# Kernel optimization log

Hardware: AMD Instinct MI355X
Metric: run time of the kernel (lower is better)

Reference implementation:

```python
import jax, jax.numpy as jnp
import numpy as np

N_NODES = 50000
N_EDGES = 800000
IN_FEATS = 128
N_HEADS = 4
OUT_FEATS = 32
NEG_SLOPE = 0.01  # F.leaky_relu default


def setup_inputs() -> dict:
    key = jax.random.key(0)
    k1, k2, k3, k4, k5, k6 = jax.random.split(key, 6)
    feat = jax.random.normal(k1, (N_NODES, IN_FEATS), dtype=jnp.float32)
    src = jax.random.randint(k2, (N_EDGES,), 0, N_NODES, dtype=jnp.int64)
    dst = jax.random.randint(k3, (N_EDGES,), 0, N_NODES, dtype=jnp.int64)
    # xavier-ish scaled params
    W_fc = jax.random.normal(k4, (IN_FEATS, N_HEADS * OUT_FEATS), dtype=jnp.float32) * 0.1
    attn_l = jax.random.normal(k5, (N_HEADS, OUT_FEATS), dtype=jnp.float32) * 0.1
    attn_r = jax.random.normal(k6, (N_HEADS, OUT_FEATS), dtype=jnp.float32) * 0.1
    return {"feat": feat, "src": src, "dst": dst, "W_fc": W_fc,
            "attn_l": attn_l, "attn_r": attn_r}


def reference(feat, src, dst, W_fc, attn_l, attn_r):
    N = feat.shape[0]
    H, D = attn_l.shape
    # fc projection -> [N, H, D]
    h = (feat @ W_fc).reshape(N, H, D)
    # per-node attention logits [N, H]
    el = jnp.einsum('nhd,hd->nh', h, attn_l)
    er = jnp.einsum('nhd,hd->nh', h, attn_r)
    # edge scores: u_add_v then leaky_relu -> [E, H]
    e = jax.nn.leaky_relu(el[src] + er[dst], NEG_SLOPE)
    # faithful to torch.softmax(e, dim=1): softmax over the HEADS axis per edge
    a = jax.nn.softmax(e, axis=1)
    # weighted messages and sum-aggregation over destination nodes
    msg = h[src] * a[:, :, None]                     # [E, H, D]
    rst = jax.ops.segment_sum(msg, dst, num_segments=N)  # [N, H, D]
    # residual: res_fc is Identity since in_feats == H*D
    rst = rst + feat.reshape(N, H, D)
    return jax.nn.elu(rst)
```

## Files before the change

kernel.cpp:

```cpp
#include <hip/hip_runtime.h>

typedef float f32x4 __attribute__((ext_vector_type(4)));
typedef __bf16 bf16x8 __attribute__((ext_vector_type(8)));
typedef unsigned short u16x4 __attribute__((ext_vector_type(4)));
typedef unsigned short u16x8 __attribute__((ext_vector_type(8)));

#define BSH 4
#define BN 16
#define CAPFIX 512
#define PNB_MAX 3200
#define PCH 4096
#define FC_ROWS 64

__device__ inline unsigned short f2bf(float x) {
  unsigned int u = __builtin_bit_cast(unsigned int, x);
  unsigned int r = (u + 0x7FFFu + ((u >> 16) & 1u)) >> 16;
  return (unsigned short)r;
}
__device__ inline float bf2f(unsigned short h) {
  unsigned int u = ((unsigned int)h) << 16;
  return __builtin_bit_cast(float, u);
}

__global__ __launch_bounds__(256) void zero_kernel(int* __restrict__ p, int n) {
  int i = blockIdx.x * 256 + threadIdx.x;
  if (i < n) p[i] = 0;
}

__device__ void partition_body(char* smem, const int* __restrict__ src,
                               const int* __restrict__ dst,
                               int* __restrict__ bcursor, int* __restrict__ tmp,
                               int E, int nbuck, int blk) {
  int* cnt = (int*)smem;
  int* lcur = cnt + PNB_MAX;
  int t = threadIdx.x;
  int base = blk * PCH;
  for (int i = t; i < nbuck; i += 256) cnt[i] = 0;
  __syncthreads();
  int rec[16];
  int bb[16];
#pragma unroll
  for (int i = 0; i < 16; ++i) {
    int e = base + t + i * 256;
    bb[i] = -1;
    if (e < E) {
      int d = dst[e];
      int b = d >> BSH;
      bb[i] = b;
      rec[i] = (src[e] & 0xFFFF) | ((d & (BN - 1)) << 16);
      atomicAdd(&cnt[b], 1);
    }
  }
  __syncthreads();
  for (int i = t; i < nbuck; i += 256) {
    int c = cnt[i];
    lcur[i] = c ? atomicAdd(&bcursor[i], c) : 0;
  }
  __syncthreads();
#pragma unroll
  for (int i = 0; i < 16; ++i) {
    if (bb[i] >= 0) {
      int p = atomicAdd(&lcur[bb[i]], 1);
      if (p < CAPFIX) tmp[(size_t)bb[i] * CAPFIX + p] = rec[i];
    }
  }
}

__device__ void fc_body(char* smem, const float* __restrict__ feat,
                        const float* __restrict__ W,
                        const float* __restrict__ al, const float* __restrict__ ar,
                        unsigned short* __restrict__ hbf,
                        float* __restrict__ el, float* __restrict__ er,
                        int N, int blk) {
  unsigned short* Wbl = (unsigned short*)smem;
  unsigned short* Albs = (unsigned short*)(smem + 32768);
  int t = threadIdx.x;
  int row0 = blk * FC_ROWS;
#pragma unroll
  for (int i = 0; i < 8; ++i) {
    int ch = i * 256 + t;
    int col = ch & 127;
    int kg = ch >> 7;
    float v[8];
#pragma unroll
    for (int j = 0; j < 8; ++j) v[j] = W[(kg * 8 + j) * 128 + col];
    int scol = col ^ ((kg & 7) << 4);
    u16x8 pk = {f2bf(v[0]), f2bf(v[1]), f2bf(v[2]), f2bf(v[3]),
                f2bf(v[4]), f2bf(v[5]), f2bf(v[6]), f2bf(v[7])};
    *(u16x8*)&Wbl[(size_t)(kg * 128 + scol) * 8] = pk;
  }
#pragma unroll
  for (int i = 0; i < 4; ++i) {
    int ch = i * 256 + t;
    int row = ch >> 4;
    int kg = ch & 15;
    int grow = row0 + row;
    f32x4 x0 = {}, x1 = {};
    if (grow < N) {
      const f32x4* fp = (const f32x4*)(feat + (size_t)grow * 128 + kg * 8);
      x0 = fp[0];
      x1 = fp[1];
    }
    int sc = kg * 64 + (row ^ kg);
    u16x8 pk = {f2bf(x0[0]), f2bf(x0[1]), f2bf(x0[2]), f2bf(x0[3]),
                f2bf(x1[0]), f2bf(x1[1]), f2bf(x1[2]), f2bf(x1[3])};
    *(u16x8*)&Albs[sc * 8] = pk;
  }
  __syncthreads();
  int w = t >> 6;
  int l = t & 63;
  int lr = l & 15;
  int lhi = l >> 4;
  f32x4 acc[8] = {};
  bf16x8 afr[4];
#pragma unroll
  for (int ks = 0; ks < 4; ++ks) {
    int kg = ks * 4 + lhi;
    int row = w * 16 + lr;
    afr[ks] = *(const bf16x8*)&Albs[(kg * 64 + (row ^ kg)) * 8];
  }
#pragma unroll
  for (int nt = 0; nt < 8; ++nt) {
#pragma unroll
    for (int ks = 0; ks < 4; ++ks) {
      int kg = ks * 4 + lhi;
      int col = nt * 16 + lr;
      int scol = col ^ ((kg & 7) << 4);
      bf16x8 b = *(const bf16x8*)&Wbl[(size_t)(kg * 128 + scol) * 8];
      acc[nt] = __builtin_amdgcn_mfma_f32_16x16x32_bf16(afr[ks], b, acc[nt], 0, 0, 0);
    }
  }
#pragma unroll
  for (int nt = 0; nt < 8; ++nt) {
#pragma unroll
    for (int r = 0; r < 4; ++r) {
      int g = row0 + w * 16 + lhi * 4 + r;
      if (g < N) hbf[(size_t)g * 128 + nt * 16 + lr] = f2bf(acc[nt][r]);
    }
  }
  f32x4 pl[4] = {}, pr[4] = {};
#pragma unroll
  for (int nt = 0; nt < 8; ++nt) {
    int hd = nt >> 1;
    float wl = al[nt * 16 + lr];
    float wr = ar[nt * 16 + lr];
#pragma unroll
    for (int r = 0; r < 4; ++r) {
      pl[r][hd] += acc[nt][r] * wl;
      pr[r][hd] += acc[nt][r] * wr;
    }
  }
#pragma unroll
  for (int off = 1; off < 16; off <<= 1) {
#pragma unroll
    for (int r = 0; r < 4; ++r) {
#pragma unroll
      for (int c = 0; c < 4; ++c) {
        pl[r][c] += __shfl_xor(pl[r][c], off);
        pr[r][c] += __shfl_xor(pr[r][c], off);
      }
    }
  }
  if (lr == 0) {
#pragma unroll
    for (int r = 0; r < 4; ++r) {
      int g = row0 + w * 16 + lhi * 4 + r;
      if (g < N) *(f32x4*)(el + (size_t)g * 4) = pl[r];
    }
  } else if (lr == 1) {
#pragma unroll
    for (int r = 0; r < 4; ++r) {
      int g = row0 + w * 16 + lhi * 4 + r;
      if (g < N) *(f32x4*)(er + (size_t)g * 4) = pr[r];
    }
  }
}

__global__ __launch_bounds__(256) void fused_pfc(const int* __restrict__ src,
                                                 const int* __restrict__ dst,
                                                 int* __restrict__ bcursor,
                                                 int* __restrict__ tmp,
                                                 const float* __restrict__ feat,
                                                 const float* __restrict__ W,
                                                 const float* __restrict__ al,
                                                 const float* __restrict__ ar,
                                                 unsigned short* __restrict__ hbf,
                                                 float* __restrict__ el,
                                                 float* __restrict__ er,
                                                 int E, int N, int nbuck, int npart) {
  __shared__ alignas(16) char smem[49152];
  if ((int)blockIdx.x < npart)
    partition_body(smem, src, dst, bcursor, tmp, E, nbuck, blockIdx.x);
  else
    fc_body(smem, feat, W, al, ar, hbf, el, er, N, blockIdx.x - npart);
}

__global__ __launch_bounds__(256) void bucket_gather(const unsigned short* __restrict__ hbf,
                                                     const float* __restrict__ el,
                                                     const float* __restrict__ er,
                                                     const int* __restrict__ bcnt,
                                                     const int* __restrict__ tmp,
                                                     const float* __restrict__ feat,
                                                     float* __restrict__ out, int N) {
  __shared__ unsigned short as_s[CAPFIX];
  __shared__ unsigned short as_a[CAPFIX * 4];
  __shared__ f32x4 er_l[BN];
  __shared__ int cnt[BN], lb[BN], lc2[BN];
  int t = threadIdx.x;
  int bkt = blockIdx.x;
  int nstart = bkt << BSH;
  if (t < BN) {
    int nd = nstart + t;
    f32x4 e4 = {};
    if (nd < N) e4 = *(const f32x4*)(er + (size_t)nd * 4);
    er_l[t] = e4;
    cnt[t] = 0;
    lc2[t] = 0;
  }
  __syncthreads();
  int nrec = min(bcnt[bkt], CAPFIX);
  int myrec[2], mydlo[2];
#pragma unroll
  for (int i = 0; i < 2; ++i) {
    int idx = t + i * 256;
    mydlo[i] = -1;
    if (idx < nrec) {
      int r = tmp[(size_t)bkt * CAPFIX + idx];
      myrec[i] = r;
      int dlo = (r >> 16) & (BN - 1);
      mydlo[i] = dlo;
      atomicAdd(&cnt[dlo], 1);
    }
  }
  __syncthreads();
  if (t < BN) {
    int v = cnt[t];
    int s = v;
#pragma unroll
    for (int o = 1; o < BN; o <<= 1) {
      int x = __shfl_up(s, o, BN);
      if (t >= o) s += x;
    }
    lb[t] = s - v;
  }
  __syncthreads();
#pragma unroll
  for (int i = 0; i < 2; ++i) {
    if (mydlo[i] >= 0) {
      int r = myrec[i];
      int s = r & 0xFFFF;
      int dlo = mydlo[i];
      int p = lb[dlo] + atomicAdd(&lc2[dlo], 1);
      f32x4 l4 = *(const f32x4*)(el + (size_t)s * 4);
      f32x4 r4 = er_l[dlo];
      float e0 = l4[0] + r4[0];
      float e1 = l4[1] + r4[1];
      float e2 = l4[2] + r4[2];
      float e3 = l4[3] + r4[3];
      e0 = e0 > 0.f ? e0 : 0.01f * e0;
      e1 = e1 > 0.f ? e1 : 0.01f * e1;
      e2 = e2 > 0.f ? e2 : 0.01f * e2;
      e3 = e3 > 0.f ? e3 : 0.01f * e3;
      float m = fmaxf(fmaxf(e0, e1), fmaxf(e2, e3));
      float a0 = __expf(e0 - m);
      float a1 = __expf(e1 - m);
      float a2 = __expf(e2 - m);
      float a3 = __expf(e3 - m);
      float inv = 1.0f / (a0 + a1 + a2 + a3);
      u16x4 a = {f2bf(a0 * inv), f2bf(a1 * inv), f2bf(a2 * inv), f2bf(a3 * inv)};
      as_s[p] = (unsigned short)s;
      *(u16x4*)&as_a[p * 4] = a;
    }
  }
  __syncthreads();
  int gid = t >> 5, lane = t & 31, head = lane >> 3;
#pragma unroll
  for (int ni = 0; ni < 2; ++ni) {
    int g = gid * 2 + ni;
    int nd = nstart + g;
    f32x4 acc = {};
    int st = lb[g], en = st + cnt[g];
    int e = st;
    for (; e + 3 < en; e += 4) {
      int s0 = as_s[e + 0];
      int s1 = as_s[e + 1];
      int s2 = as_s[e + 2];
      int s3 = as_s[e + 3];
      float a0 = bf2f(as_a[(e + 0) * 4 + head]);
      float a1 = bf2f(as_a[(e + 1) * 4 + head]);
      float a2 = bf2f(as_a[(e + 2) * 4 + head]);
      float a3 = bf2f(as_a[(e + 3) * 4 + head]);
      u16x4 v0 = *(const u16x4*)&hbf[(size_t)s0 * 128 + lane * 4];
      u16x4 v1 = *(const u16x4*)&hbf[(size_t)s1 * 128 + lane * 4];
      u16x4 v2 = *(const u16x4*)&hbf[(size_t)s2 * 128 + lane * 4];
      u16x4 v3 = *(const u16x4*)&hbf[(size_t)s3 * 128 + lane * 4];
      f32x4 h0 = {bf2f(v0[0]), bf2f(v0[1]), bf2f(v0[2]), bf2f(v0[3])};
      f32x4 h1 = {bf2f(v1[0]), bf2f(v1[1]), bf2f(v1[2]), bf2f(v1[3])};
      f32x4 h2 = {bf2f(v2[0]), bf2f(v2[1]), bf2f(v2[2]), bf2f(v2[3])};
      f32x4 h3 = {bf2f(v3[0]), bf2f(v3[1]), bf2f(v3[2]), bf2f(v3[3])};
      acc += h0 * a0;
      acc += h1 * a1;
      acc += h2 * a2;
      acc += h3 * a3;
    }
    for (; e < en; ++e) {
      int s0 = as_s[e];
      float a0 = bf2f(as_a[e * 4 + head]);
      u16x4 v0 = *(const u16x4*)&hbf[(size_t)s0 * 128 + lane * 4];
      f32x4 h0 = {bf2f(v0[0]), bf2f(v0[1]), bf2f(v0[2]), bf2f(v0[3])};
      acc += h0 * a0;
    }
    if (nd < N) {
      f32x4 f = *(const f32x4*)(feat + (size_t)nd * 128 + lane * 4);
      f32x4 o = acc + f;
#pragma unroll
      for (int c = 0; c < 4; ++c) o[c] = o[c] > 0.f ? o[c] : expm1f(o[c]);
      *(f32x4*)(out + (size_t)nd * 128 + lane * 4) = o;
    }
  }
}

extern "C" void kernel_launch(void* const* d_in, const int* in_sizes, int n_in,
                              void* d_out, int out_size, void* d_ws, size_t ws_size,
                              hipStream_t stream) {
  const float* feat = (const float*)d_in[0];
  const int* src = (const int*)d_in[1];
  const int* dst = (const int*)d_in[2];
  const float* W = (const float*)d_in[3];
  const float* al = (const float*)d_in[4];
  const float* ar = (const float*)d_in[5];
  float* out = (float*)d_out;

  int N = in_sizes[0] / 128;
  int E = in_sizes[1];
  int nbuck = (N + BN - 1) >> BSH;

  char* p = (char*)d_ws;
  unsigned short* hbf = (unsigned short*)p; p += (size_t)N * 128 * 2;
  float* el = (float*)p; p += (size_t)N * 4 * 4;
  float* er = (float*)p; p += (size_t)N * 4 * 4;
  int* bcursor = (int*)p; p += (size_t)((nbuck + 3) & ~3) * 4;
  int* tmp = (int*)p;

  int npart = (E + PCH - 1) / PCH;
  int nfc = (N + FC_ROWS - 1) / FC_ROWS;

  zero_kernel<<<(nbuck + 255) / 256, 256, 0, stream>>>(bcursor, nbuck);
  fused_pfc<<<npart + nfc, 256, 0, stream>>>(src, dst, bcursor, tmp, feat, W, al, ar,
                                             hbf, el, er, E, N, nbuck, npart);
  bucket_gather<<<nbuck, 256, 0, stream>>>(hbf, el, er, bcursor, tmp, feat, out, N);
}
```

Baseline: 71.98 us.

## Precompute bf16 weights once and widen gather to full-wave rows

The bf16 conversion of W moves into the zeroing kernel, which writes it once to a workspace buffer. The FC blocks then read W fragments straight from global/L2 instead of each block converting and staging it in LDS, which frees LDS and may raise occupancy. The gather stage now maps one 64-lane wave per node row with 2 features per lane, instead of 32 lanes with 4 features. It also preloads the residual into the accumulator. This trades shared-memory staging for repeated global reads of W, and narrower per-lane loads for more nodes handled per wave.

```diff
diff --git a/kernel.cpp b/kernel.cpp
--- a/kernel.cpp
+++ b/kernel.cpp
@@ -1,7 +1,9 @@
 #include <hip/hip_runtime.h>
 
+typedef float f32x2 __attribute__((ext_vector_type(2)));
 typedef float f32x4 __attribute__((ext_vector_type(4)));
 typedef __bf16 bf16x8 __attribute__((ext_vector_type(8)));
+typedef unsigned short u16x2 __attribute__((ext_vector_type(2)));
 typedef unsigned short u16x4 __attribute__((ext_vector_type(4)));
 typedef unsigned short u16x8 __attribute__((ext_vector_type(8)));
 
@@ -22,9 +24,24 @@
   return __builtin_bit_cast(float, u);
 }
 
-__global__ __launch_bounds__(256) void zero_kernel(int* __restrict__ p, int n) {
-  int i = blockIdx.x * 256 + threadIdx.x;
-  if (i < n) p[i] = 0;
+__global__ __launch_bounds__(256) void prezero_kernel(const float* __restrict__ W,
+                                                      unsigned short* __restrict__ wtp,
+                                                      int* __restrict__ bcursor, int n) {
+  int b = blockIdx.x;
+  if (b < 8) {
+    int tid = b * 256 + threadIdx.x;
+    int col = tid & 127;
+    int kg = tid >> 7;
+    float v[8];
+#pragma unroll
+    for (int j = 0; j < 8; ++j) v[j] = W[(kg * 8 + j) * 128 + col];
+    u16x8 pk = {f2bf(v[0]), f2bf(v[1]), f2bf(v[2]), f2bf(v[3]),
+                f2bf(v[4]), f2bf(v[5]), f2bf(v[6]), f2bf(v[7])};
+    *(u16x8*)&wtp[(size_t)(kg * 128 + col) * 8] = pk;
+  } else {
+    int i = (b - 8) * 256 + threadIdx.x;
+    if (i < n) bcursor[i] = 0;
+  }
 }
 
 __device__ void partition_body(char* smem, const int* __restrict__ src,
@@ -67,28 +84,14 @@
 }
 
 __device__ void fc_body(char* smem, const float* __restrict__ feat,
-                        const float* __restrict__ W,
+                        const unsigned short* __restrict__ wtp,
                         const float* __restrict__ al, const float* __restrict__ ar,
                         unsigned short* __restrict__ hbf,
                         float* __restrict__ el, float* __restrict__ er,
                         int N, int blk) {
-  unsigned short* Wbl = (unsigned short*)smem;
-  unsigned short* Albs = (unsigned short*)(smem + 32768);
+  unsigned short* Albs = (unsigned short*)smem;
   int t = threadIdx.x;
   int row0 = blk * FC_ROWS;
-#pragma unroll
-  for (int i = 0; i < 8; ++i) {
-    int ch = i * 256 + t;
-    int col = ch & 127;
-    int kg = ch >> 7;
-    float v[8];
-#pragma unroll
-    for (int j = 0; j < 8; ++j) v[j] = W[(kg * 8 + j) * 128 + col];
-    int scol = col ^ ((kg & 7) << 4);
-    u16x8 pk = {f2bf(v[0]), f2bf(v[1]), f2bf(v[2]), f2bf(v[3]),
-                f2bf(v[4]), f2bf(v[5]), f2bf(v[6]), f2bf(v[7])};
-    *(u16x8*)&Wbl[(size_t)(kg * 128 + scol) * 8] = pk;
-  }
 #pragma unroll
   for (int i = 0; i < 4; ++i) {
     int ch = i * 256 + t;
@@ -125,8 +128,7 @@
     for (int ks = 0; ks < 4; ++ks) {
       int kg = ks * 4 + lhi;
       int col = nt * 16 + lr;
-      int scol = col ^ ((kg & 7) << 4);
-      bf16x8 b = *(const bf16x8*)&Wbl[(size_t)(kg * 128 + scol) * 8];
+      bf16x8 b = *(const bf16x8*)&wtp[(size_t)(kg * 128 + col) * 8];
       acc[nt] = __builtin_amdgcn_mfma_f32_16x16x32_bf16(afr[ks], b, acc[nt], 0, 0, 0);
     }
   }
@@ -181,18 +183,18 @@
                                                  int* __restrict__ bcursor,
                                                  int* __restrict__ tmp,
                                                  const float* __restrict__ feat,
-                                                 const float* __restrict__ W,
+                                                 const unsigned short* __restrict__ wtp,
                                                  const float* __restrict__ al,
                                                  const float* __restrict__ ar,
                                                  unsigned short* __restrict__ hbf,
                                                  float* __restrict__ el,
                                                  float* __restrict__ er,
                                                  int E, int N, int nbuck, int npart) {
-  __shared__ alignas(16) char smem[49152];
+  __shared__ alignas(16) char smem[PNB_MAX * 8];
   if ((int)blockIdx.x < npart)
     partition_body(smem, src, dst, bcursor, tmp, E, nbuck, blockIdx.x);
   else
-    fc_body(smem, feat, W, al, ar, hbf, el, er, N, blockIdx.x - npart);
+    fc_body(smem, feat, wtp, al, ar, hbf, el, er, N, blockIdx.x - npart);
 }
 
 __global__ __launch_bounds__(256) void bucket_gather(const unsigned short* __restrict__ hbf,
@@ -273,12 +275,15 @@
     }
   }
   __syncthreads();
-  int gid = t >> 5, lane = t & 31, head = lane >> 3;
-#pragma unroll
-  for (int ni = 0; ni < 2; ++ni) {
-    int g = gid * 2 + ni;
+  int wv = t >> 6;
+  int lane = t & 63;
+  int head = lane >> 4;
+#pragma unroll
+  for (int ni = 0; ni < 4; ++ni) {
+    int g = wv * 4 + ni;
     int nd = nstart + g;
-    f32x4 acc = {};
+    f32x2 acc = {};
+    if (nd < N) acc = *(const f32x2*)(feat + (size_t)nd * 128 + lane * 2);
     int st = lb[g], en = st + cnt[g];
     int e = st;
     for (; e + 3 < en; e += 4) {
@@ -290,14 +295,14 @@
       float a1 = bf2f(as_a[(e + 1) * 4 + head]);
       float a2 = bf2f(as_a[(e + 2) * 4 + head]);
       float a3 = bf2f(as_a[(e + 3) * 4 + head]);
-      u16x4 v0 = *(const u16x4*)&hbf[(size_t)s0 * 128 + lane * 4];
-      u16x4 v1 = *(const u16x4*)&hbf[(size_t)s1 * 128 + lane * 4];
-      u16x4 v2 = *(const u16x4*)&hbf[(size_t)s2 * 128 + lane * 4];
-      u16x4 v3 = *(const u16x4*)&hbf[(size_t)s3 * 128 + lane * 4];
-      f32x4 h0 = {bf2f(v0[0]), bf2f(v0[1]), bf2f(v0[2]), bf2f(v0[3])};
-      f32x4 h1 = {bf2f(v1[0]), bf2f(v1[1]), bf2f(v1[2]), bf2f(v1[3])};
-      f32x4 h2 = {bf2f(v2[0]), bf2f(v2[1]), bf2f(v2[2]), bf2f(v2[3])};
-      f32x4 h3 = {bf2f(v3[0]), bf2f(v3[1]), bf2f(v3[2]), bf2f(v3[3])};
+      u16x2 v0 = *(const u16x2*)&hbf[(size_t)s0 * 128 + lane * 2];
+      u16x2 v1 = *(const u16x2*)&hbf[(size_t)s1 * 128 + lane * 2];
+      u16x2 v2 = *(const u16x2*)&hbf[(size_t)s2 * 128 + lane * 2];
+      u16x2 v3 = *(const u16x2*)&hbf[(size_t)s3 * 128 + lane * 2];
+      f32x2 h0 = {bf2f(v0[0]), bf2f(v0[1])};
+      f32x2 h1 = {bf2f(v1[0]), bf2f(v1[1])};
+      f32x2 h2 = {bf2f(v2[0]), bf2f(v2[1])};
+      f32x2 h3 = {bf2f(v3[0]), bf2f(v3[1])};
       acc += h0 * a0;
       acc += h1 * a1;
       acc += h2 * a2;
@@ -306,16 +311,15 @@
     for (; e < en; ++e) {
       int s0 = as_s[e];
       float a0 = bf2f(as_a[e * 4 + head]);
-      u16x4 v0 = *(const u16x4*)&hbf[(size_t)s0 * 128 + lane * 4];
-      f32x4 h0 = {bf2f(v0[0]), bf2f(v0[1]), bf2f(v0[2]), bf2f(v0[3])};
+      u16x2 v0 = *(const u16x2*)&hbf[(size_t)s0 * 128 + lane * 2];
+      f32x2 h0 = {bf2f(v0[0]), bf2f(v0[1])};
       acc += h0 * a0;
     }
     if (nd < N) {
-      f32x4 f = *(const f32x4*)(feat + (size_t)nd * 128 + lane * 4);
-      f32x4 o = acc + f;
-#pragma unroll
-      for (int c = 0; c < 4; ++c) o[c] = o[c] > 0.f ? o[c] : expm1f(o[c]);
-      *(f32x4*)(out + (size_t)nd * 128 + lane * 4) = o;
+      f32x2 o = acc;
+      o[0] = o[0] > 0.f ? o[0] : expm1f(o[0]);
+      o[1] = o[1] > 0.f ? o[1] : expm1f(o[1]);
+      *(f32x2*)(out + (size_t)nd * 128 + lane * 2) = o;
     }
   }
 }
@@ -339,14 +343,15 @@
   unsigned short* hbf = (unsigned short*)p; p += (size_t)N * 128 * 2;
   float* el = (float*)p; p += (size_t)N * 4 * 4;
   float* er = (float*)p; p += (size_t)N * 4 * 4;
+  unsigned short* wtp = (unsigned short*)p; p += 2048 * 16;
   int* bcursor = (int*)p; p += (size_t)((nbuck + 3) & ~3) * 4;
   int* tmp = (int*)p;
 
   int npart = (E + PCH - 1) / PCH;
   int nfc = (N + FC_ROWS - 1) / FC_ROWS;
 
-  zero_kernel<<<(nbuck + 255) / 256, 256, 0, stream>>>(bcursor, nbuck);
-  fused_pfc<<<npart + nfc, 256, 0, stream>>>(src, dst, bcursor, tmp, feat, W, al, ar,
+  prezero_kernel<<<8 + (nbuck + 255) / 256, 256, 0, stream>>>(W, wtp, bcursor, nbuck);
+  fused_pfc<<<npart + nfc, 256, 0, stream>>>(src, dst, bcursor, tmp, feat, wtp, al, ar,
                                              hbf, el, er, E, N, nbuck, npart);
   bucket_gather<<<nbuck, 256, 0, stream>>>(hbf, el, er, bcursor, tmp, feat, out, N);
 }
```

After: 72.75 us. Within noise of the previous version (+1.1%).
